# Optimization experiments

Measured on AMD Instinct MI355X. Metric: run time of the kernel, lower is better.

The kernel has to match this reference:

```python
import jax, jax.numpy as jnp
import numpy as np

B, T, N, C, H = 64, 12, 1370, 8, 64

def setup_inputs() -> dict:
    key = jax.random.key(0)
    ks = jax.random.split(key, 7)
    s_ih = 1.0 / np.sqrt(H)
    inp = {
        "x": jax.random.normal(ks[0], (B, T, N, C), dtype=jnp.float32),
        # PyTorch nn.LSTM params, gate order (i, f, g, o)
        "W_ih": jax.random.uniform(ks[1], (4 * H, C), jnp.float32, -s_ih, s_ih),
        "W_hh": jax.random.uniform(ks[2], (4 * H, H), jnp.float32, -s_ih, s_ih),
        "b_ih": jax.random.uniform(ks[3], (4 * H,), jnp.float32, -s_ih, s_ih),
        "b_hh": jax.random.uniform(ks[4], (4 * H,), jnp.float32, -s_ih, s_ih),
        "W_fc": jax.random.uniform(ks[5], (C, H), jnp.float32, -s_ih, s_ih),
        "b_fc": jax.random.uniform(ks[6], (C,), jnp.float32, -s_ih, s_ih),
    }
    return inp

def reference(x, W_ih, W_hh, b_ih, b_hh, W_fc, b_fc):
    Bx, Tx, Nx, Cx = x.shape
    Hh = W_hh.shape[1]
    # (B, T, N, C) -> (B*N, T, C): shared-weight LSTM over all node sequences
    xr = jnp.transpose(x, (0, 2, 1, 3)).reshape(Bx * Nx, Tx, Cx)
    # Precompute input projections for all timesteps: (B*N, T, 4H)
    x_gates = jnp.einsum('btc,gc->btg', xr, W_ih) + b_ih
    # time-major for scan: (T, B*N, 4H)
    x_gates = jnp.moveaxis(x_gates, 1, 0)

    def step(carry, xg):
        h, c = carry
        gates = xg + h @ W_hh.T + b_hh  # (B*N, 4H)
        i, f, g, o = jnp.split(gates, 4, axis=-1)
        i = jax.nn.sigmoid(i)
        f = jax.nn.sigmoid(f)
        g = jnp.tanh(g)
        o = jax.nn.sigmoid(o)
        c = f * c + i * g
        h = o * jnp.tanh(c)
        return (h, c), None

    h0 = jnp.zeros((Bx * Nx, Hh), dtype=x.dtype)
    c0 = jnp.zeros((Bx * Nx, Hh), dtype=x.dtype)
    (h_last, _), _ = jax.lax.scan(step, (h0, c0), x_gates)

    y_flat = h_last @ W_fc.T + b_fc  # (B*N, C)
    return y_flat.reshape(Bx, Nx, Cx)
```

## Files before the change

### kernel.cpp

```cpp
#include <hip/hip_runtime.h>

#define T_ 12
#define N_ 1370
#define MSEQ 64
#define LDA 72
#define NBLK 1370
#define NFRAG 48

typedef __attribute__((ext_vector_type(8))) short short8;
typedef __attribute__((ext_vector_type(4))) float floatx4;
typedef __attribute__((ext_vector_type(4))) unsigned uint4v;
typedef __attribute__((ext_vector_type(2))) unsigned uint2v;

#define NLOG2E -1.4426950408889634f
#define TLOG2E 2.8853900817779268f
#define N2LOG2E -5.7707801635558536f

__device__ __forceinline__ short f2bf(float x) {
  unsigned u = __builtin_bit_cast(unsigned, x);
  u = (u + 0x7fffu + ((u >> 16) & 1u)) >> 16;
  return (short)u;
}
__device__ __forceinline__ unsigned pk_bf16(float a, float b) {
  unsigned r;
  asm("v_cvt_pk_bf16_f32 %0, %1, %2" : "=v"(r) : "v"(a), "v"(b));
  return r;
}
__device__ __forceinline__ short8 load_w8s(const float* __restrict__ p, float s) {
  floatx4 a = *(const floatx4*)p;
  floatx4 b = *(const floatx4*)(p + 4);
  uint4v u = {pk_bf16(a[0] * s, a[1] * s), pk_bf16(a[2] * s, a[3] * s),
              pk_bf16(b[0] * s, b[1] * s), pk_bf16(b[2] * s, b[3] * s)};
  return __builtin_bit_cast(short8, u);
}

__global__ void __launch_bounds__(256, 2) lstm_kernel(
    const float* __restrict__ x, const float* __restrict__ W_ih,
    const float* __restrict__ W_hh, const float* __restrict__ b_ih,
    const float* __restrict__ b_hh, const float* __restrict__ W_fc,
    const float* __restrict__ b_fc, float* __restrict__ out) {
  __shared__ short wlds[NFRAG][64][8];
  __shared__ short hstrip[4][2][16][LDA];
  __shared__ __align__(16) short xbuf[T_][MSEQ][8];
  __shared__ __align__(16) short ones_row[8];

  const int tid = threadIdx.x;
  const int wave = tid >> 6;
  const int lane = tid & 63;
  const int m16 = lane & 15;
  const int q = lane >> 4;
  const int blk = blockIdx.x;

#pragma unroll
  for (int i = 0; i < 12; ++i) {
    const int fid = wave * 12 + i;
    short8 v = {0, 0, 0, 0, 0, 0, 0, 0};
    if (fid < 32) {
      const int gu = fid >> 1, kc = fid & 1;
      const int g = gu >> 2, ut = gu & 3;
      const float sg = (g == 2) ? TLOG2E : NLOG2E;
      const int grow = g * 64 + ut * 16 + m16;
      v = load_w8s(W_hh + grow * 64 + kc * 32 + q * 8, sg);
    } else {
      const int gu = fid - 32;
      const int g = gu >> 2, ut = gu & 3;
      const float sg = (g == 2) ? TLOG2E : NLOG2E;
      const int grow = g * 64 + ut * 16 + m16;
      if (q == 0) {
        v = load_w8s(W_ih + grow * 8, sg);
      } else if (q == 1) {
        v[0] = f2bf(sg * (b_ih[grow] + b_hh[grow]));
      }
    }
    *(short8*)&wlds[fid][lane][0] = v;
  }

  {
    int* hp = (int*)hstrip;
#pragma unroll
    for (int i = tid; i < (int)(sizeof(hstrip) / 4); i += 256) hp[i] = 0;
    if (tid < 8) ones_row[tid] = (tid == 0) ? (short)0x3F80 : (short)0;
  }

  {
#pragma unroll
    for (int j = 0; j < 6; ++j) {
      const int slot = j * 256 + tid;
      const int t = slot >> 7;
      const int idx = slot & 127;
      const int seq = idx >> 1;
      const int half = idx & 1;
      const int s0 = blk * MSEQ + seq;
      const int bidx = s0 / N_;
      const int nidx = s0 - bidx * N_;
      const floatx4 v = *(const floatx4*)(
          x + (((size_t)bidx * T_ + t) * N_ + nidx) * 8 + half * 4);
      uint2v u = {pk_bf16(v[0], v[1]), pk_bf16(v[2], v[3])};
      *(uint2v*)&xbuf[t][seq][half * 4] = u;
    }
  }
  __syncthreads();

  short8 wA[4][4][2];
#pragma unroll
  for (int g = 0; g < 4; ++g)
#pragma unroll
    for (int ut = 0; ut < 4; ++ut)
#pragma unroll
      for (int kc = 0; kc < 2; ++kc)
        wA[g][ut][kc] =
            *(const short8*)&wlds[(((g << 2) | ut) << 1) | kc][lane][0];

  const floatx4 zacc = {0.0f, 0.0f, 0.0f, 0.0f};

  float cst[4][4];
#pragma unroll
  for (int ut = 0; ut < 4; ++ut)
#pragma unroll
    for (int r = 0; r < 4; ++r) cst[ut][r] = 0.0f;

#pragma unroll 2
  for (int t = 0; t < T_; ++t) {
    const int rb = t & 1, wb = rb ^ 1;
    short8 b0 = *(const short8*)&hstrip[wave][rb][m16][q * 8];
    short8 b1 = *(const short8*)&hstrip[wave][rb][m16][32 + q * 8];
    const short* bxp = q ? &ones_row[0] : &xbuf[t][wave * 16 + m16][0];
    short8 bx = *(const short8*)bxp;
#pragma unroll
    for (int ut = 0; ut < 4; ++ut) {
      short8 wx0 = *(const short8*)&wlds[32 + ut][lane][0];
      short8 wx1 = *(const short8*)&wlds[36 + ut][lane][0];
      short8 wx2 = *(const short8*)&wlds[40 + ut][lane][0];
      short8 wx3 = *(const short8*)&wlds[44 + ut][lane][0];
      floatx4 gi = __builtin_amdgcn_mfma_f32_16x16x32_bf16(wA[0][ut][0], b0, zacc, 0, 0, 0);
      floatx4 gf = __builtin_amdgcn_mfma_f32_16x16x32_bf16(wA[1][ut][0], b0, zacc, 0, 0, 0);
      floatx4 gg = __builtin_amdgcn_mfma_f32_16x16x32_bf16(wA[2][ut][0], b0, zacc, 0, 0, 0);
      floatx4 go = __builtin_amdgcn_mfma_f32_16x16x32_bf16(wA[3][ut][0], b0, zacc, 0, 0, 0);
      gi = __builtin_amdgcn_mfma_f32_16x16x32_bf16(wA[0][ut][1], b1, gi, 0, 0, 0);
      gf = __builtin_amdgcn_mfma_f32_16x16x32_bf16(wA[1][ut][1], b1, gf, 0, 0, 0);
      gg = __builtin_amdgcn_mfma_f32_16x16x32_bf16(wA[2][ut][1], b1, gg, 0, 0, 0);
      go = __builtin_amdgcn_mfma_f32_16x16x32_bf16(wA[3][ut][1], b1, go, 0, 0, 0);
      gi = __builtin_amdgcn_mfma_f32_16x16x32_bf16(wx0, bx, gi, 0, 0, 0);
      gf = __builtin_amdgcn_mfma_f32_16x16x32_bf16(wx1, bx, gf, 0, 0, 0);
      gg = __builtin_amdgcn_mfma_f32_16x16x32_bf16(wx2, bx, gg, 0, 0, 0);
      go = __builtin_amdgcn_mfma_f32_16x16x32_bf16(wx3, bx, go, 0, 0, 0);
      float hv[4];
#pragma unroll
      for (int r = 0; r < 4; ++r) {
        float di = 1.0f + __builtin_amdgcn_exp2f(gi[r]);
        float df = 1.0f + __builtin_amdgcn_exp2f(gf[r]);
        float dg = 1.0f + __builtin_amdgcn_exp2f(gg[r]);
        float dq = 1.0f + __builtin_amdgcn_exp2f(go[r]);
        float pa = di * df, pb = dg * dq;
        float rp = __builtin_amdgcn_rcpf(pa * pb);
        float fv = rp * di * pb;
        float rpa = rp * pa;
        float ov = rpa * dg;
        float tg = fmaf(TLOG2E, dg, N2LOG2E);
        float ig = tg * rp * (df * dq);
        float cs = fmaf(fv, cst[ut][r], ig);
        cst[ut][r] = cs;
        float dt = 1.0f + __builtin_amdgcn_exp2f(cs);
        float tc = fmaf(-2.0f, __builtin_amdgcn_rcpf(dt), 1.0f);
        hv[r] = ov * tc;
      }
      unsigned long long pk =
          (unsigned long long)pk_bf16(hv[0], hv[1]) |
          ((unsigned long long)pk_bf16(hv[2], hv[3]) << 32);
      *(unsigned long long*)&hstrip[wave][wb][m16][ut * 16 + q * 4] = pk;
    }
  }

  {
    short8 f0, f1;
    short8 z = {0, 0, 0, 0, 0, 0, 0, 0};
    if (m16 < 8) {
      const float* wr = W_fc + m16 * 64;
      f0 = load_w8s(wr + q * 8, 1.0f);
      f1 = load_w8s(wr + 32 + q * 8, 1.0f);
    } else {
      f0 = z;
      f1 = z;
    }
    short8 h0 = *(const short8*)&hstrip[wave][0][m16][q * 8];
    short8 h1 = *(const short8*)&hstrip[wave][0][m16][32 + q * 8];
    floatx4 acc = __builtin_amdgcn_mfma_f32_16x16x32_bf16(f0, h0, zacc, 0, 0, 0);
    acc = __builtin_amdgcn_mfma_f32_16x16x32_bf16(f1, h1, acc, 0, 0, 0);
    if (q < 2) {
      const int orow = blk * MSEQ + wave * 16 + m16;
#pragma unroll
      for (int r = 0; r < 4; ++r)
        out[orow * 8 + q * 4 + r] = acc[r] + b_fc[q * 4 + r];
    }
  }
}

extern "C" void kernel_launch(void* const* d_in, const int* in_sizes, int n_in,
                              void* d_out, int out_size, void* d_ws,
                              size_t ws_size, hipStream_t stream) {
  const float* x    = (const float*)d_in[0];
  const float* W_ih = (const float*)d_in[1];
  const float* W_hh = (const float*)d_in[2];
  const float* b_ih = (const float*)d_in[3];
  const float* b_hh = (const float*)d_in[4];
  const float* W_fc = (const float*)d_in[5];
  const float* b_fc = (const float*)d_in[6];
  float* out = (float*)d_out;
  hipLaunchKernelGGL(lstm_kernel, dim3(NBLK), dim3(256), 0, stream,
                     x, W_ih, W_hh, b_ih, b_hh, W_fc, b_fc, out);
}
```

Before: 172.5 us.

## Keep hidden state in registers via 16x16x16 MFMA layout, drop LDS h round-trip

```diff
diff --git a/kernel.cpp b/kernel.cpp
--- a/kernel.cpp
+++ b/kernel.cpp
@@ -2,15 +2,13 @@
 
 #define T_ 12
 #define N_ 1370
-#define MSEQ 64
-#define LDA 72
 #define NBLK 1370
-#define NFRAG 48
-
+
+typedef __attribute__((ext_vector_type(4))) short short4v;
 typedef __attribute__((ext_vector_type(8))) short short8;
 typedef __attribute__((ext_vector_type(4))) float floatx4;
+typedef __attribute__((ext_vector_type(2))) unsigned uint2v;
 typedef __attribute__((ext_vector_type(4))) unsigned uint4v;
-typedef __attribute__((ext_vector_type(2))) unsigned uint2v;
 
 #define NLOG2E -1.4426950408889634f
 #define TLOG2E 2.8853900817779268f
@@ -26,23 +24,42 @@
   asm("v_cvt_pk_bf16_f32 %0, %1, %2" : "=v"(r) : "v"(a), "v"(b));
   return r;
 }
-__device__ __forceinline__ short8 load_w8s(const float* __restrict__ p, float s) {
-  floatx4 a = *(const floatx4*)p;
-  floatx4 b = *(const floatx4*)(p + 4);
-  uint4v u = {pk_bf16(a[0] * s, a[1] * s), pk_bf16(a[2] * s, a[3] * s),
-              pk_bf16(b[0] * s, b[1] * s), pk_bf16(b[2] * s, b[3] * s)};
-  return __builtin_bit_cast(short8, u);
-}
-
-__global__ void __launch_bounds__(256, 2) lstm_kernel(
+__device__ __forceinline__ uint2v cvt4(const float* __restrict__ p, float s) {
+  floatx4 v = *(const floatx4*)p;
+  uint2v r = {pk_bf16(v[0] * s, v[1] * s), pk_bf16(v[2] * s, v[3] * s)};
+  return r;
+}
+__device__ __forceinline__ short4v mk4(unsigned lo, unsigned hi) {
+  uint2v u = {lo, hi};
+  return __builtin_bit_cast(short4v, u);
+}
+__device__ __forceinline__ short4v lo4(short8 v) {
+  return __builtin_shufflevector(v, v, 0, 1, 2, 3);
+}
+__device__ __forceinline__ short4v hi4(short8 v) {
+  return __builtin_shufflevector(v, v, 4, 5, 6, 7);
+}
+
+__device__ __forceinline__ floatx4 mfma16(short4v a, short4v b, floatx4 c) {
+#if __has_builtin(__builtin_amdgcn_mfma_f32_16x16x16bf16_1k)
+  return __builtin_amdgcn_mfma_f32_16x16x16bf16_1k(a, b, c, 0, 0, 0);
+#elif __has_builtin(__builtin_amdgcn_mfma_f32_16x16x16_bf16)
+  return __builtin_amdgcn_mfma_f32_16x16x16_bf16(a, b, c, 0, 0, 0);
+#else
+  asm volatile("v_mfma_f32_16x16x16_bf16 %0, %1, %2, %0\n\ts_nop 7\n\ts_nop 7"
+               : "+v"(c)
+               : "v"(a), "v"(b));
+  return c;
+#endif
+}
+
+__global__ void __launch_bounds__(256, 4) lstm_kernel(
     const float* __restrict__ x, const float* __restrict__ W_ih,
     const float* __restrict__ W_hh, const float* __restrict__ b_ih,
     const float* __restrict__ b_hh, const float* __restrict__ W_fc,
     const float* __restrict__ b_fc, float* __restrict__ out) {
-  __shared__ short wlds[NFRAG][64][8];
-  __shared__ short hstrip[4][2][16][LDA];
-  __shared__ __align__(16) short xbuf[T_][MSEQ][8];
-  __shared__ __align__(16) short ones_row[8];
+  __shared__ short8 whl[32][64];
+  __shared__ short4v wxl[16][64];
 
   const int tid = threadIdx.x;
   const int wave = tid >> 6;
@@ -52,66 +69,49 @@
   const int blk = blockIdx.x;
 
 #pragma unroll
-  for (int i = 0; i < 12; ++i) {
-    const int fid = wave * 12 + i;
-    short8 v = {0, 0, 0, 0, 0, 0, 0, 0};
-    if (fid < 32) {
-      const int gu = fid >> 1, kc = fid & 1;
-      const int g = gu >> 2, ut = gu & 3;
-      const float sg = (g == 2) ? TLOG2E : NLOG2E;
-      const int grow = g * 64 + ut * 16 + m16;
-      v = load_w8s(W_hh + grow * 64 + kc * 32 + q * 8, sg);
-    } else {
-      const int gu = fid - 32;
-      const int g = gu >> 2, ut = gu & 3;
-      const float sg = (g == 2) ? TLOG2E : NLOG2E;
-      const int grow = g * 64 + ut * 16 + m16;
-      if (q == 0) {
-        v = load_w8s(W_ih + grow * 8, sg);
-      } else if (q == 1) {
-        v[0] = f2bf(sg * (b_ih[grow] + b_hh[grow]));
-      }
-    }
-    *(short8*)&wlds[fid][lane][0] = v;
-  }
-
-  {
-    int* hp = (int*)hstrip;
-#pragma unroll
-    for (int i = tid; i < (int)(sizeof(hstrip) / 4); i += 256) hp[i] = 0;
-    if (tid < 8) ones_row[tid] = (tid == 0) ? (short)0x3F80 : (short)0;
-  }
-
-  {
-#pragma unroll
-    for (int j = 0; j < 6; ++j) {
-      const int slot = j * 256 + tid;
-      const int t = slot >> 7;
-      const int idx = slot & 127;
-      const int seq = idx >> 1;
-      const int half = idx & 1;
-      const int s0 = blk * MSEQ + seq;
-      const int bidx = s0 / N_;
-      const int nidx = s0 - bidx * N_;
-      const floatx4 v = *(const floatx4*)(
-          x + (((size_t)bidx * T_ + t) * N_ + nidx) * 8 + half * 4);
-      uint2v u = {pk_bf16(v[0], v[1]), pk_bf16(v[2], v[3])};
-      *(uint2v*)&xbuf[t][seq][half * 4] = u;
-    }
+  for (int p = 0; p < 8; ++p) {
+    const int s = p * 256 + tid;
+    const int l = s & 63, f = s >> 6;
+    const int g = f >> 3, ut = (f >> 1) & 3, kc2 = f & 1;
+    const float sg = (g == 2) ? TLOG2E : NLOG2E;
+    const int md = l & 15, qd = l >> 4;
+    const float* wr = W_hh + (g * 64 + ut * 16 + md) * 64 + kc2 * 32 + qd * 4;
+    uint2v w0 = cvt4(wr, sg);
+    uint2v w1 = cvt4(wr + 16, sg);
+    uint4v u = {w0.x, w0.y, w1.x, w1.y};
+    whl[f][l] = __builtin_bit_cast(short8, u);
+  }
+#pragma unroll
+  for (int p = 0; p < 4; ++p) {
+    const int s = p * 256 + tid;
+    const int l = s & 63, f = s >> 6;
+    const int g = f >> 2, ut = f & 3;
+    const float sg = (g == 2) ? TLOG2E : NLOG2E;
+    const int md = l & 15, qd = l >> 4;
+    const int grow = g * 64 + ut * 16 + md;
+    uint2v w = {0u, 0u};
+    if (qd < 2) {
+      w = cvt4(W_ih + grow * 8 + qd * 4, sg);
+    } else if (qd == 2) {
+      w.x = (unsigned)(unsigned short)f2bf(sg * (b_ih[grow] + b_hh[grow]));
+    }
+    wxl[f][l] = __builtin_bit_cast(short4v, w);
   }
   __syncthreads();
 
-  short8 wA[4][4][2];
-#pragma unroll
-  for (int g = 0; g < 4; ++g)
-#pragma unroll
-    for (int ut = 0; ut < 4; ++ut)
-#pragma unroll
-      for (int kc = 0; kc < 2; ++kc)
-        wA[g][ut][kc] =
-            *(const short8*)&wlds[(((g << 2) | ut) << 1) | kc][lane][0];
+  const int seq = blk * 64 + wave * 16 + m16;
+  const int bidx = seq / N_;
+  const int nidx = seq - bidx * N_;
+  const float* xptr = x + ((size_t)(bidx * T_) * N_ + nidx) * 8 + q * 4;
+  const size_t xstride = (size_t)N_ * 8;
+
+  floatx4 cx = {0.0f, 0.0f, 0.0f, 0.0f};
+  if (q < 2) cx = *(const floatx4*)xptr;
 
   const floatx4 zacc = {0.0f, 0.0f, 0.0f, 0.0f};
+  short4v hA[4];
+#pragma unroll
+  for (int kc = 0; kc < 4; ++kc) hA[kc] = mk4(0u, 0u);
 
   float cst[4][4];
 #pragma unroll
@@ -121,41 +121,40 @@
 
 #pragma unroll 2
   for (int t = 0; t < T_; ++t) {
-    const int rb = t & 1, wb = rb ^ 1;
-    short8 b0 = *(const short8*)&hstrip[wave][rb][m16][q * 8];
-    short8 b1 = *(const short8*)&hstrip[wave][rb][m16][32 + q * 8];
-    const short* bxp = q ? &ones_row[0] : &xbuf[t][wave * 16 + m16][0];
-    short8 bx = *(const short8*)bxp;
+    uint2v xw = {pk_bf16(cx[0], cx[1]), pk_bf16(cx[2], cx[3])};
+    if (q == 2) xw.x = 0x00003F80u;
+    const short4v xB = __builtin_bit_cast(short4v, xw);
+    floatx4 nx = {0.0f, 0.0f, 0.0f, 0.0f};
+    if (t + 1 < T_ && q < 2)
+      nx = *(const floatx4*)(xptr + (size_t)(t + 1) * xstride);
+
+    short4v hN[4];
 #pragma unroll
     for (int ut = 0; ut < 4; ++ut) {
-      short8 wx0 = *(const short8*)&wlds[32 + ut][lane][0];
-      short8 wx1 = *(const short8*)&wlds[36 + ut][lane][0];
-      short8 wx2 = *(const short8*)&wlds[40 + ut][lane][0];
-      short8 wx3 = *(const short8*)&wlds[44 + ut][lane][0];
-      floatx4 gi = __builtin_amdgcn_mfma_f32_16x16x32_bf16(wA[0][ut][0], b0, zacc, 0, 0, 0);
-      floatx4 gf = __builtin_amdgcn_mfma_f32_16x16x32_bf16(wA[1][ut][0], b0, zacc, 0, 0, 0);
-      floatx4 gg = __builtin_amdgcn_mfma_f32_16x16x32_bf16(wA[2][ut][0], b0, zacc, 0, 0, 0);
-      floatx4 go = __builtin_amdgcn_mfma_f32_16x16x32_bf16(wA[3][ut][0], b0, zacc, 0, 0, 0);
-      gi = __builtin_amdgcn_mfma_f32_16x16x32_bf16(wA[0][ut][1], b1, gi, 0, 0, 0);
-      gf = __builtin_amdgcn_mfma_f32_16x16x32_bf16(wA[1][ut][1], b1, gf, 0, 0, 0);
-      gg = __builtin_amdgcn_mfma_f32_16x16x32_bf16(wA[2][ut][1], b1, gg, 0, 0, 0);
-      go = __builtin_amdgcn_mfma_f32_16x16x32_bf16(wA[3][ut][1], b1, go, 0, 0, 0);
-      gi = __builtin_amdgcn_mfma_f32_16x16x32_bf16(wx0, bx, gi, 0, 0, 0);
-      gf = __builtin_amdgcn_mfma_f32_16x16x32_bf16(wx1, bx, gf, 0, 0, 0);
-      gg = __builtin_amdgcn_mfma_f32_16x16x32_bf16(wx2, bx, gg, 0, 0, 0);
-      go = __builtin_amdgcn_mfma_f32_16x16x32_bf16(wx3, bx, go, 0, 0, 0);
+      floatx4 acc[4];
+#pragma unroll
+      for (int g = 0; g < 4; ++g) {
+        const short8 pA = whl[(g * 4 + ut) * 2 + 0][lane];
+        const short8 pB = whl[(g * 4 + ut) * 2 + 1][lane];
+        const short4v ax = wxl[g * 4 + ut][lane];
+        floatx4 c = mfma16(lo4(pA), hA[0], zacc);
+        c = mfma16(hi4(pA), hA[1], c);
+        c = mfma16(lo4(pB), hA[2], c);
+        c = mfma16(hi4(pB), hA[3], c);
+        c = mfma16(ax, xB, c);
+        acc[g] = c;
+      }
       float hv[4];
 #pragma unroll
       for (int r = 0; r < 4; ++r) {
-        float di = 1.0f + __builtin_amdgcn_exp2f(gi[r]);
-        float df = 1.0f + __builtin_amdgcn_exp2f(gf[r]);
-        float dg = 1.0f + __builtin_amdgcn_exp2f(gg[r]);
-        float dq = 1.0f + __builtin_amdgcn_exp2f(go[r]);
+        float di = 1.0f + __builtin_amdgcn_exp2f(acc[0][r]);
+        float df = 1.0f + __builtin_amdgcn_exp2f(acc[1][r]);
+        float dg = 1.0f + __builtin_amdgcn_exp2f(acc[2][r]);
+        float dq = 1.0f + __builtin_amdgcn_exp2f(acc[3][r]);
         float pa = di * df, pb = dg * dq;
         float rp = __builtin_amdgcn_rcpf(pa * pb);
         float fv = rp * di * pb;
-        float rpa = rp * pa;
-        float ov = rpa * dg;
+        float ov = rp * pa * dg;
         float tg = fmaf(TLOG2E, dg, N2LOG2E);
         float ig = tg * rp * (df * dq);
         float cs = fmaf(fv, cst[ut][r], ig);
@@ -164,30 +163,26 @@
         float tc = fmaf(-2.0f, __builtin_amdgcn_rcpf(dt), 1.0f);
         hv[r] = ov * tc;
       }
-      unsigned long long pk =
-          (unsigned long long)pk_bf16(hv[0], hv[1]) |
-          ((unsigned long long)pk_bf16(hv[2], hv[3]) << 32);
-      *(unsigned long long*)&hstrip[wave][wb][m16][ut * 16 + q * 4] = pk;
-    }
+      hN[ut] = mk4(pk_bf16(hv[0], hv[1]), pk_bf16(hv[2], hv[3]));
+    }
+#pragma unroll
+    for (int kc = 0; kc < 4; ++kc) hA[kc] = hN[kc];
+    cx = nx;
   }
 
   {
-    short8 f0, f1;
-    short8 z = {0, 0, 0, 0, 0, 0, 0, 0};
-    if (m16 < 8) {
-      const float* wr = W_fc + m16 * 64;
-      f0 = load_w8s(wr + q * 8, 1.0f);
-      f1 = load_w8s(wr + 32 + q * 8, 1.0f);
-    } else {
-      f0 = z;
-      f1 = z;
-    }
-    short8 h0 = *(const short8*)&hstrip[wave][0][m16][q * 8];
-    short8 h1 = *(const short8*)&hstrip[wave][0][m16][32 + q * 8];
-    floatx4 acc = __builtin_amdgcn_mfma_f32_16x16x32_bf16(f0, h0, zacc, 0, 0, 0);
-    acc = __builtin_amdgcn_mfma_f32_16x16x32_bf16(f1, h1, acc, 0, 0, 0);
+    short4v fcA[4];
+#pragma unroll
+    for (int kc = 0; kc < 4; ++kc) {
+      uint2v w = {0u, 0u};
+      if (m16 < 8) w = cvt4(W_fc + m16 * 64 + kc * 16 + q * 4, 1.0f);
+      fcA[kc] = __builtin_bit_cast(short4v, w);
+    }
+    floatx4 acc = zacc;
+#pragma unroll
+    for (int kc = 0; kc < 4; ++kc) acc = mfma16(fcA[kc], hA[kc], acc);
     if (q < 2) {
-      const int orow = blk * MSEQ + wave * 16 + m16;
+      const int orow = blk * 64 + wave * 16 + m16;
 #pragma unroll
       for (int r = 0; r < 4; ++r)
         out[orow * 8 + q * 4 + r] = acc[r] + b_fc[q * 4 + r];
```

After: 432.9 us. 2.51x slower.
